# Optimization experiments

Measured on AMD Instinct MI355X. Metric: run time of the kernel, lower is better.

## Reference

```python
import jax, jax.numpy as jnp
import numpy as np

# Norse default neuron parameters
DT = 0.001
TAU_SYN_INV = 200.0
TAU_MEM_INV = 100.0
V_TH = 1.0  # v_leak = v_reset = 0
ALPHA = 100.0  # SuperSpike surrogate slope


@jax.custom_vjp
def heaviside(x):
    return (x > 0).astype(x.dtype)

def _h_fwd(x):
    return heaviside(x), x

def _h_bwd(x, g):
    # SuperSpike surrogate gradient: 1 / (alpha*|x| + 1)^2
    return (g / (ALPHA * jnp.abs(x) + 1.0) ** 2,)

heaviside.defvjp(_h_fwd, _h_bwd)


def setup_inputs() -> dict:
    key = jax.random.key(0)
    k0, k1, k2, k3 = jax.random.split(key, 4)
    T, B, NI, NF, NO = 1000, 64, 700, 1024, 20
    x = jax.random.normal(k0, (T, B, NI), jnp.float32)
    w_in = jax.random.normal(k1, (NF, NI), jnp.float32) / np.sqrt(NI)
    w_rec = jax.random.normal(k2, (NF, NF), jnp.float32) / np.sqrt(NF)
    w_out = jax.random.normal(k3, (NO, NF), jnp.float32) / np.sqrt(NF)
    return {"x": x, "w_in": w_in, "w_rec": w_rec, "w_out": w_out}


def reference(x, w_in, w_rec, w_out):
    # x: [T, B, NI]
    T, B, NI = x.shape
    NF = w_in.shape[0]
    NO = w_out.shape[0]
    z0 = jnp.zeros((B, NF), x.dtype)
    v0 = jnp.zeros((B, NF), x.dtype)
    i0 = jnp.zeros((B, NF), x.dtype)
    vo0 = jnp.zeros((B, NO), x.dtype)
    io0 = jnp.zeros((B, NO), x.dtype)

    def step(carry, xt):
        z, v, i, vo, io = carry
        # --- recurrent LIF cell (lif_step) ---
        i_dec = i * (1.0 - DT * TAU_SYN_INV)          # synaptic current decay
        v_dec = v + DT * TAU_MEM_INV * (-v + i)       # membrane integration (v_leak=0)
        z_new = heaviside(v_dec - V_TH)               # spike
        v_new = (1.0 - z_new) * v_dec                 # reset to v_reset=0 on spike
        i_new = i_dec + xt @ w_in.T + z @ w_rec.T     # input + recurrence (prev z)
        # --- LI readout cell (li_step) ---
        io_dec = io * (1.0 - DT * TAU_SYN_INV)
        vo_new = vo + DT * TAU_MEM_INV * (-vo + io)
        io_new = io_dec + z_new @ w_out.T
        return (z_new, v_new, i_new, vo_new, io_new), None

    (zf, vf, i_f, vof, iof), _ = jax.lax.scan(step, (z0, v0, i0, vo0, io0), x)
    return jax.nn.log_softmax(vof, axis=1)
```

## Files before the change

### kernel.cpp

```cpp
#include <hip/hip_runtime.h>
#include <cstdint>
#include <cstddef>

#define T_STEPS 1000
#define BATCH   64
#define NI_DIM  700
#define NF_DIM  1024
#define NO_DIM  20
#define M_DIM   (T_STEPS * BATCH)

#define XW_OFF    0ull
#define WRT_OFF   (XW_OFF + 65536000ull)
#define WINT_OFF  (WRT_OFF + 1048576ull)
#define WOUTT_OFF (WINT_OFF + 716800ull)
#define FLAGS_OFF (WOUTT_OFF + 20480ull)
#define WS_FLOATS (FLAGS_OFF + 512ull)

#define REC_WGS  64
#define GBM 128
#define GBN 256
#define GBK 16
#define MT_TILES (M_DIM / GBM)
#define NT_TILES (NF_DIM / GBN)
#define SMEM_BYTES 25088

typedef float vfloat4 __attribute__((ext_vector_type(4)));

__global__ void transpose_k(const float* __restrict__ src, float* __restrict__ dst,
                            int R, int C) {
  __shared__ float tile[32][33];
  int c0 = blockIdx.x * 32, r0 = blockIdx.y * 32;
  int x = threadIdx.x, y = threadIdx.y;
#pragma unroll
  for (int j = 0; j < 32; j += 8) {
    int r = r0 + y + j, c = c0 + x;
    if (r < R && c < C) tile[y + j][x] = src[(size_t)r * C + c];
  }
  __syncthreads();
#pragma unroll
  for (int j = 0; j < 32; j += 8) {
    int r = r0 + x, c = c0 + y + j;
    if (c < C && r < R) dst[(size_t)c * R + r] = tile[x][y + j];
  }
}

__global__ void zero_flags_k(int* __restrict__ flags) {
  if (threadIdx.x < 512) flags[threadIdx.x] = 0;
}

__global__ __launch_bounds__(1024) void fused_k(
    const float* __restrict__ x, const float* __restrict__ w_inT,
    float* __restrict__ XW, const float* __restrict__ wrT,
    const float* __restrict__ w_outT, int* __restrict__ flags,
    float* __restrict__ out) {
  __shared__ __attribute__((aligned(16))) char smem[SMEM_BYTES];
  const int tid = threadIdx.x;

  if (blockIdx.x >= REC_WGS) {
    float (*As)[GBM + 4] = reinterpret_cast<float (*)[GBM + 4]>(smem);
    float (*Bs)[GBN + 4] =
        reinterpret_cast<float (*)[GBN + 4]>(smem + GBK * (GBM + 4) * 4);
    const int id = blockIdx.x - REC_WGS;
    const int mt = id >> 2;
    const int nt = id & 3;
    const int m0 = mt * GBM, n0 = nt * GBN;
    const int tx = tid & 31, ty = tid >> 5;

    float acc[4][8];
#pragma unroll
    for (int i = 0; i < 4; ++i)
#pragma unroll
      for (int j = 0; j < 8; ++j) acc[i][j] = 0.f;

    for (int k0 = 0; k0 < NI_DIM; k0 += GBK) {
      {
        int ar = tid >> 3, ac = (tid & 7) * 2;
        const float* src = x + (size_t)(m0 + ar) * NI_DIM + k0 + ac;
        float v0 = (k0 + ac     < NI_DIM) ? __builtin_nontemporal_load(src)     : 0.f;
        float v1 = (k0 + ac + 1 < NI_DIM) ? __builtin_nontemporal_load(src + 1) : 0.f;
        As[ac][ar] = v0;
        As[ac + 1][ar] = v1;
      }
      {
        int r = tid >> 6, c4 = (tid & 63) * 4;
        int kk = k0 + r;
        float4 vv = make_float4(0.f, 0.f, 0.f, 0.f);
        if (kk < NI_DIM)
          vv = *reinterpret_cast<const float4*>(w_inT + (size_t)kk * NF_DIM + n0 + c4);
        *reinterpret_cast<float4*>(&Bs[r][c4]) = vv;
      }
      __syncthreads();
#pragma unroll
      for (int k = 0; k < GBK; ++k) {
        float a[4], b[8];
#pragma unroll
        for (int i = 0; i < 4; ++i) a[i] = As[k][ty * 4 + i];
#pragma unroll
        for (int j = 0; j < 8; ++j) b[j] = Bs[k][tx * 8 + j];
#pragma unroll
        for (int i = 0; i < 4; ++i)
#pragma unroll
          for (int j = 0; j < 8; ++j) acc[i][j] += a[i] * b[j];
      }
      __syncthreads();
    }

#pragma unroll
    for (int i = 0; i < 4; ++i) {
      size_t row = (size_t)(m0 + ty * 4 + i);
      float* cp = XW + row * NF_DIM + n0 + tx * 8;
      vfloat4 v0 = {acc[i][0], acc[i][1], acc[i][2], acc[i][3]};
      vfloat4 v1 = {acc[i][4], acc[i][5], acc[i][6], acc[i][7]};
      __builtin_nontemporal_store(v0, reinterpret_cast<vfloat4*>(cp));
      __builtin_nontemporal_store(v1, reinterpret_cast<vfloat4*>(cp + 4));
    }
    __syncthreads();
    if (tid == 0)
      __hip_atomic_fetch_add(&flags[mt], 1, __ATOMIC_RELEASE,
                             __HIP_MEMORY_SCOPE_AGENT);
    return;
  }

  {
#pragma clang fp contract(off)
    int*   s_flat = reinterpret_cast<int*>(smem);
    int*   s_wcnt = reinterpret_cast<int*>(smem + 8192);
    float* s_part = reinterpret_cast<float*>(smem + 8320);
    float* s_vo   = reinterpret_cast<float*>(smem + 10880);

    const int b = blockIdx.x;
    const int lane = tid & 63, wid = tid >> 6;
    const unsigned tidu = (unsigned)tid;

    float v = 0.f, cur = 0.f;
    float vo = 0.f, io = 0.f;
    int C = 0;

    const float* xwp = XW + (size_t)b * NF_DIM + tid;

    if (tid == 0) {
      while (__hip_atomic_load(&flags[0], __ATOMIC_RELAXED,
                               __HIP_MEMORY_SCOPE_AGENT) < NT_TILES)
        __builtin_amdgcn_s_sleep(2);
      (void)__hip_atomic_load(&flags[0], __ATOMIC_ACQUIRE,
                              __HIP_MEMORY_SCOPE_AGENT);
    }
    __syncthreads();

    for (int t = 0; t < T_STEPS; ++t) {
      const int pn = t & 1, po = pn ^ 1;
      float xwv = __builtin_nontemporal_load(xwp + (size_t)t * (BATCH * NF_DIM));

      const int* fl = s_flat + po * NF_DIM;
      float rec = 0.f;
      int kk = 0;
      for (; kk + 32 <= C; kk += 32) {
        int idx[32];
#pragma unroll
        for (int u = 0; u < 8; ++u)
          *reinterpret_cast<int4*>(&idx[u * 4]) =
              *reinterpret_cast<const int4*>(&fl[kk + u * 4]);
        float val[32];
#pragma unroll
        for (int u = 0; u < 32; ++u)
          val[u] = wrT[(((unsigned)idx[u]) << 10) + tidu];
#pragma unroll
        for (int u = 0; u < 32; ++u) rec += val[u];
      }
      for (; kk + 8 <= C; kk += 8) {
        int idx[8];
#pragma unroll
        for (int u = 0; u < 2; ++u)
          *reinterpret_cast<int4*>(&idx[u * 4]) =
              *reinterpret_cast<const int4*>(&fl[kk + u * 4]);
        float val[8];
#pragma unroll
        for (int u = 0; u < 8; ++u)
          val[u] = wrT[(((unsigned)idx[u]) << 10) + tidu];
#pragma unroll
        for (int u = 0; u < 8; ++u) rec += val[u];
      }
      for (; kk < C; ++kk) rec += wrT[(((unsigned)fl[kk]) << 10) + tidu];

      float i_dec = cur * 0.8f;
      float v_dec = v + 0.1f * (cur - v);
      bool  z     = v_dec > 1.0f;
      v   = z ? 0.f : v_dec;
      cur = (i_dec + xwv) + rec;

      unsigned long long m = __ballot(z);
      int pos = __popcll(m & ((1ull << lane) - 1ull));
      if (lane == 0) s_wcnt[pn * 16 + wid] = __popcll(m);

      if (lane < NO_DIM) {
        float p = 0.f;
        unsigned long long mm = m;
        while (mm) {
          int bset = __builtin_ctzll(mm);
          mm &= mm - 1;
          p += w_outT[((wid << 6) + bset) * NO_DIM + lane];
        }
        s_part[(pn * 16 + wid) * NO_DIM + lane] = p;
      }

      __syncthreads();

      int total = 0, myoff = 0;
#pragma unroll
      for (int w = 0; w < 16; ++w) {
        int c = s_wcnt[pn * 16 + w];
        if (w < wid) myoff += c;
        total += c;
      }
      if (z) s_flat[pn * NF_DIM + myoff + pos] = tid;
      C = total;

      if (tid < NO_DIM) {
        float io_dec = io * 0.8f;
        vo = vo + 0.1f * (io - vo);
        float acc = 0.f;
#pragma unroll
        for (int w = 0; w < 16; ++w) acc += s_part[(pn * 16 + w) * NO_DIM + tid];
        io = io_dec + acc;
      }

      if ((t & 1) && (t + 1 < T_STEPS) && tid == 0) {
        const int c = (t + 1) >> 1;
        while (__hip_atomic_load(&flags[c], __ATOMIC_RELAXED,
                                 __HIP_MEMORY_SCOPE_AGENT) < NT_TILES)
          __builtin_amdgcn_s_sleep(2);
        (void)__hip_atomic_load(&flags[c], __ATOMIC_ACQUIRE,
                                __HIP_MEMORY_SCOPE_AGENT);
      }
      __syncthreads();
    }

    if (tid < NO_DIM) s_vo[tid] = vo;
    __syncthreads();
    if (tid < NO_DIM) {
      float mx = -3.402823466e+38f;
      for (int j = 0; j < NO_DIM; ++j) mx = fmaxf(mx, s_vo[j]);
      float sum = 0.f;
      for (int j = 0; j < NO_DIM; ++j) sum += expf(s_vo[j] - mx);
      out[(size_t)b * NO_DIM + tid] = (vo - mx) - logf(sum);
    }
  }
}

extern "C" void kernel_launch(void* const* d_in, const int* in_sizes, int n_in,
                              void* d_out, int out_size, void* d_ws, size_t ws_size,
                              hipStream_t stream) {
  const float* x     = (const float*)d_in[0];
  const float* w_in  = (const float*)d_in[1];
  const float* w_rec = (const float*)d_in[2];
  const float* w_out = (const float*)d_in[3];
  float* out = (float*)d_out;
  float* ws  = (float*)d_ws;

  if (ws_size < WS_FLOATS * sizeof(float)) return;

  float* xw    = ws + XW_OFF;
  float* wrT   = ws + WRT_OFF;
  float* w_inT = ws + WINT_OFF;
  float* w_oT  = ws + WOUTT_OFF;
  int*   flags = (int*)(ws + FLAGS_OFF);

  {
    dim3 blk(32, 8);
    dim3 g1((NI_DIM + 31) / 32, (NF_DIM + 31) / 32);
    transpose_k<<<g1, blk, 0, stream>>>(w_in, w_inT, NF_DIM, NI_DIM);
    dim3 g2((NF_DIM + 31) / 32, (NF_DIM + 31) / 32);
    transpose_k<<<g2, blk, 0, stream>>>(w_rec, wrT, NF_DIM, NF_DIM);
    dim3 g3((NF_DIM + 31) / 32, (NO_DIM + 31) / 32);
    transpose_k<<<g3, blk, 0, stream>>>(w_out, w_oT, NO_DIM, NF_DIM);
    zero_flags_k<<<1, 512, 0, stream>>>(flags);
  }

  fused_k<<<REC_WGS + MT_TILES * NT_TILES, 1024, 0, stream>>>(
      x, w_inT, xw, wrT, w_oT, flags, out);
}
```

Before: 3.475 ms.

## Halve workgroup size to 512 threads with two neurons per thread

Launches the fused kernel with 512-thread workgroups (launch bounds 512,4). In the recurrent part each thread now handles two neurons (tid and tid+512), issuing both gathers per spike index. In the GEMM part each thread computes an 8x8 tile with strided column access. The intent is to cut per-step barrier cost across fewer waves, raise GEMM work per thread, and allow more workgroups per CU. The cost is higher register pressure, and the spike-list ordering and readout reduction change to match.

```diff
diff --git a/kernel.cpp b/kernel.cpp
--- a/kernel.cpp
+++ b/kernel.cpp
@@ -48,7 +48,7 @@
   if (threadIdx.x < 512) flags[threadIdx.x] = 0;
 }
 
-__global__ __launch_bounds__(1024) void fused_k(
+__global__ __launch_bounds__(512, 4) void fused_k(
     const float* __restrict__ x, const float* __restrict__ w_inT,
     float* __restrict__ XW, const float* __restrict__ wrT,
     const float* __restrict__ w_outT, int* __restrict__ flags,
@@ -64,41 +64,48 @@
     const int mt = id >> 2;
     const int nt = id & 3;
     const int m0 = mt * GBM, n0 = nt * GBN;
-    const int tx = tid & 31, ty = tid >> 5;
-
-    float acc[4][8];
-#pragma unroll
-    for (int i = 0; i < 4; ++i)
+    const int tx = tid & 31;
+    const int ty = tid >> 5;
+
+    float acc[8][8];
+#pragma unroll
+    for (int i = 0; i < 8; ++i)
 #pragma unroll
       for (int j = 0; j < 8; ++j) acc[i][j] = 0.f;
 
     for (int k0 = 0; k0 < NI_DIM; k0 += GBK) {
       {
-        int ar = tid >> 3, ac = (tid & 7) * 2;
+        int ar = tid >> 2, ac = (tid & 3) * 4;
         const float* src = x + (size_t)(m0 + ar) * NI_DIM + k0 + ac;
-        float v0 = (k0 + ac     < NI_DIM) ? __builtin_nontemporal_load(src)     : 0.f;
-        float v1 = (k0 + ac + 1 < NI_DIM) ? __builtin_nontemporal_load(src + 1) : 0.f;
-        As[ac][ar] = v0;
-        As[ac + 1][ar] = v1;
+#pragma unroll
+        for (int u = 0; u < 4; ++u) {
+          float vv = (k0 + ac + u < NI_DIM) ? __builtin_nontemporal_load(src + u) : 0.f;
+          As[ac + u][ar] = vv;
+        }
       }
       {
-        int r = tid >> 6, c4 = (tid & 63) * 4;
+        int r = tid >> 5, c8 = (tid & 31) * 8;
         int kk = k0 + r;
-        float4 vv = make_float4(0.f, 0.f, 0.f, 0.f);
-        if (kk < NI_DIM)
-          vv = *reinterpret_cast<const float4*>(w_inT + (size_t)kk * NF_DIM + n0 + c4);
-        *reinterpret_cast<float4*>(&Bs[r][c4]) = vv;
+        float4 v0 = make_float4(0.f, 0.f, 0.f, 0.f);
+        float4 v1 = make_float4(0.f, 0.f, 0.f, 0.f);
+        if (kk < NI_DIM) {
+          const float* bp = w_inT + (size_t)kk * NF_DIM + n0 + c8;
+          v0 = *reinterpret_cast<const float4*>(bp);
+          v1 = *reinterpret_cast<const float4*>(bp + 4);
+        }
+        *reinterpret_cast<float4*>(&Bs[r][c8]) = v0;
+        *reinterpret_cast<float4*>(&Bs[r][c8 + 4]) = v1;
       }
       __syncthreads();
 #pragma unroll
       for (int k = 0; k < GBK; ++k) {
-        float a[4], b[8];
-#pragma unroll
-        for (int i = 0; i < 4; ++i) a[i] = As[k][ty * 4 + i];
-#pragma unroll
-        for (int j = 0; j < 8; ++j) b[j] = Bs[k][tx * 8 + j];
-#pragma unroll
-        for (int i = 0; i < 4; ++i)
+        float a[8], b[8];
+#pragma unroll
+        for (int i = 0; i < 8; ++i) a[i] = As[k][ty * 8 + i];
+#pragma unroll
+        for (int j = 0; j < 8; ++j) b[j] = Bs[k][tx + 32 * j];
+#pragma unroll
+        for (int i = 0; i < 8; ++i)
 #pragma unroll
           for (int j = 0; j < 8; ++j) acc[i][j] += a[i] * b[j];
       }
@@ -106,13 +113,12 @@
     }
 
 #pragma unroll
-    for (int i = 0; i < 4; ++i) {
-      size_t row = (size_t)(m0 + ty * 4 + i);
-      float* cp = XW + row * NF_DIM + n0 + tx * 8;
-      vfloat4 v0 = {acc[i][0], acc[i][1], acc[i][2], acc[i][3]};
-      vfloat4 v1 = {acc[i][4], acc[i][5], acc[i][6], acc[i][7]};
-      __builtin_nontemporal_store(v0, reinterpret_cast<vfloat4*>(cp));
-      __builtin_nontemporal_store(v1, reinterpret_cast<vfloat4*>(cp + 4));
+    for (int i = 0; i < 8; ++i) {
+      size_t row = (size_t)(m0 + ty * 8 + i);
+      float* cp = XW + row * NF_DIM + n0 + tx;
+#pragma unroll
+      for (int j = 0; j < 8; ++j)
+        __builtin_nontemporal_store(acc[i][j], cp + 32 * j);
     }
     __syncthreads();
     if (tid == 0)
@@ -126,13 +132,15 @@
     int*   s_flat = reinterpret_cast<int*>(smem);
     int*   s_wcnt = reinterpret_cast<int*>(smem + 8192);
     float* s_part = reinterpret_cast<float*>(smem + 8320);
-    float* s_vo   = reinterpret_cast<float*>(smem + 10880);
+    float* s_vo   = reinterpret_cast<float*>(smem + 9600);
 
     const int b = blockIdx.x;
     const int lane = tid & 63, wid = tid >> 6;
-    const unsigned tidu = (unsigned)tid;
-
-    float v = 0.f, cur = 0.f;
+    const unsigned n0u = (unsigned)tid;
+    const unsigned n1u = (unsigned)tid + 512;
+
+    float v0 = 0.f, cur0 = 0.f;
+    float v1 = 0.f, cur1 = 0.f;
     float vo = 0.f, io = 0.f;
     int C = 0;
 
@@ -149,10 +157,12 @@
 
     for (int t = 0; t < T_STEPS; ++t) {
       const int pn = t & 1, po = pn ^ 1;
-      float xwv = __builtin_nontemporal_load(xwp + (size_t)t * (BATCH * NF_DIM));
+      const float* xt = xwp + (size_t)t * (BATCH * NF_DIM);
+      float xwv0 = __builtin_nontemporal_load(xt);
+      float xwv1 = __builtin_nontemporal_load(xt + 512);
 
       const int* fl = s_flat + po * NF_DIM;
-      float rec = 0.f;
+      float recA = 0.f, recB = 0.f;
       int kk = 0;
       for (; kk + 32 <= C; kk += 32) {
         int idx[32];
@@ -160,12 +170,17 @@
         for (int u = 0; u < 8; ++u)
           *reinterpret_cast<int4*>(&idx[u * 4]) =
               *reinterpret_cast<const int4*>(&fl[kk + u * 4]);
-        float val[32];
-#pragma unroll
-        for (int u = 0; u < 32; ++u)
-          val[u] = wrT[(((unsigned)idx[u]) << 10) + tidu];
-#pragma unroll
-        for (int u = 0; u < 32; ++u) rec += val[u];
+        float valA[32], valB[32];
+#pragma unroll
+        for (int u = 0; u < 32; ++u) {
+          const float* rp = wrT + (((unsigned)idx[u]) << 10);
+          valA[u] = rp[n0u];
+          valB[u] = rp[n1u];
+        }
+#pragma unroll
+        for (int u = 0; u < 32; ++u) recA += valA[u];
+#pragma unroll
+        for (int u = 0; u < 32; ++u) recB += valB[u];
       }
       for (; kk + 8 <= C; kk += 8) {
         int idx[8];
@@ -173,46 +188,75 @@
         for (int u = 0; u < 2; ++u)
           *reinterpret_cast<int4*>(&idx[u * 4]) =
               *reinterpret_cast<const int4*>(&fl[kk + u * 4]);
-        float val[8];
-#pragma unroll
-        for (int u = 0; u < 8; ++u)
-          val[u] = wrT[(((unsigned)idx[u]) << 10) + tidu];
-#pragma unroll
-        for (int u = 0; u < 8; ++u) rec += val[u];
-      }
-      for (; kk < C; ++kk) rec += wrT[(((unsigned)fl[kk]) << 10) + tidu];
-
-      float i_dec = cur * 0.8f;
-      float v_dec = v + 0.1f * (cur - v);
-      bool  z     = v_dec > 1.0f;
-      v   = z ? 0.f : v_dec;
-      cur = (i_dec + xwv) + rec;
-
-      unsigned long long m = __ballot(z);
-      int pos = __popcll(m & ((1ull << lane) - 1ull));
-      if (lane == 0) s_wcnt[pn * 16 + wid] = __popcll(m);
+        float valA[8], valB[8];
+#pragma unroll
+        for (int u = 0; u < 8; ++u) {
+          const float* rp = wrT + (((unsigned)idx[u]) << 10);
+          valA[u] = rp[n0u];
+          valB[u] = rp[n1u];
+        }
+#pragma unroll
+        for (int u = 0; u < 8; ++u) recA += valA[u];
+#pragma unroll
+        for (int u = 0; u < 8; ++u) recB += valB[u];
+      }
+      for (; kk < C; ++kk) {
+        const float* rp = wrT + (((unsigned)fl[kk]) << 10);
+        recA += rp[n0u];
+        recB += rp[n1u];
+      }
+
+      float i_dec0 = cur0 * 0.8f;
+      float v_dec0 = v0 + 0.1f * (cur0 - v0);
+      bool  z0     = v_dec0 > 1.0f;
+      v0   = z0 ? 0.f : v_dec0;
+      cur0 = (i_dec0 + xwv0) + recA;
+
+      float i_dec1 = cur1 * 0.8f;
+      float v_dec1 = v1 + 0.1f * (cur1 - v1);
+      bool  z1     = v_dec1 > 1.0f;
+      v1   = z1 ? 0.f : v_dec1;
+      cur1 = (i_dec1 + xwv1) + recB;
+
+      unsigned long long m0 = __ballot(z0);
+      unsigned long long m1 = __ballot(z1);
+      unsigned long long ltmask = (1ull << lane) - 1ull;
+      int pos0 = __popcll(m0 & ltmask);
+      int pos1 = __popcll(m1 & ltmask);
+      if (lane == 0) {
+        s_wcnt[pn * 16 + wid]     = __popcll(m0);
+        s_wcnt[pn * 16 + 8 + wid] = __popcll(m1);
+      }
 
       if (lane < NO_DIM) {
         float p = 0.f;
-        unsigned long long mm = m;
+        unsigned long long mm = m0;
         while (mm) {
           int bset = __builtin_ctzll(mm);
           mm &= mm - 1;
           p += w_outT[((wid << 6) + bset) * NO_DIM + lane];
         }
-        s_part[(pn * 16 + wid) * NO_DIM + lane] = p;
+        mm = m1;
+        while (mm) {
+          int bset = __builtin_ctzll(mm);
+          mm &= mm - 1;
+          p += w_outT[((512 + (wid << 6)) + bset) * NO_DIM + lane];
+        }
+        s_part[(pn * 8 + wid) * NO_DIM + lane] = p;
       }
 
       __syncthreads();
 
-      int total = 0, myoff = 0;
-#pragma unroll
-      for (int w = 0; w < 16; ++w) {
-        int c = s_wcnt[pn * 16 + w];
-        if (w < wid) myoff += c;
+      int total = 0, off0 = 0, off1 = 0;
+#pragma unroll
+      for (int s = 0; s < 16; ++s) {
+        int c = s_wcnt[pn * 16 + s];
+        if (s < wid)     off0 += c;
+        if (s < 8 + wid) off1 += c;
         total += c;
       }
-      if (z) s_flat[pn * NF_DIM + myoff + pos] = tid;
+      if (z0) s_flat[pn * NF_DIM + off0 + pos0] = tid;
+      if (z1) s_flat[pn * NF_DIM + off1 + pos1] = tid + 512;
       C = total;
 
       if (tid < NO_DIM) {
@@ -220,7 +264,7 @@
         vo = vo + 0.1f * (io - vo);
         float acc = 0.f;
 #pragma unroll
-        for (int w = 0; w < 16; ++w) acc += s_part[(pn * 16 + w) * NO_DIM + tid];
+        for (int w = 0; w < 8; ++w) acc += s_part[(pn * 8 + w) * NO_DIM + tid];
         io = io_dec + acc;
       }
 
@@ -276,6 +320,6 @@
     zero_flags_k<<<1, 512, 0, stream>>>(flags);
   }
 
-  fused_k<<<REC_WGS + MT_TILES * NT_TILES, 1024, 0, stream>>>(
+  fused_k<<<REC_WGS + MT_TILES * NT_TILES, 512, 0, stream>>>(
       x, w_inT, xw, wrT, w_oT, flags, out);
 }
```

After: 5.092 ms. +46.5%, slower.
